# Optimization experiments

Measured on AMD Instinct MI355X. Metric: run time of the kernel, lower is better.

## Reference

```python
import jax, jax.numpy as jnp
import numpy as np

N = 20000      # nodes
E = 320000     # edges
F = 128        # feat_dim
N_RBF = 20
CUTOFF = 5.0


def setup_inputs() -> dict:
    key = jax.random.key(0)
    ks = jax.random.split(key, 12)
    h_i = jax.random.normal(ks[0], (N, F), dtype=jnp.float32)
    v_i = jax.random.normal(ks[1], (N, F, 3), dtype=jnp.float32)
    # distances in (0, cutoff); keep strictly > 0 to avoid div-by-zero in sinc basis
    d_ij = (jax.random.uniform(ks[2], (E,), dtype=jnp.float32) * 0.98 + 0.01) * CUTOFF
    r = jax.random.normal(ks[3], (E, 3), dtype=jnp.float32)
    unit_r_ij = r / jnp.linalg.norm(r, axis=-1, keepdims=True)
    nbrs = jax.random.randint(ks[4], (E, 2), 0, N, dtype=jnp.int64)
    # params: layers = Dense(F->F, swish) then Dense(F->3F); dist_embed dense: n_rbf -> 3F
    s1 = 1.0 / np.sqrt(F)
    W1 = jax.random.uniform(ks[5], (F, F), jnp.float32, -s1, s1)
    b1 = jax.random.uniform(ks[6], (F,), jnp.float32, -s1, s1)
    W2 = jax.random.uniform(ks[7], (F, 3 * F), jnp.float32, -s1, s1)
    b2 = jax.random.uniform(ks[8], (3 * F,), jnp.float32, -s1, s1)
    sr = 1.0 / np.sqrt(N_RBF)
    Wr = jax.random.uniform(ks[9], (N_RBF, 3 * F), jnp.float32, -sr, sr)
    br = jax.random.uniform(ks[10], (3 * F,), jnp.float32, -sr, sr)
    return {"h_i": h_i, "v_i": v_i, "d_ij": d_ij, "unit_r_ij": unit_r_ij,
            "nbrs": nbrs, "W1": W1, "b1": b1, "W2": W2, "b2": b2, "Wr": Wr, "br": br}


def _dist_embed(d, Wr, br):
    # PaiNN sinc-like radial basis: sin(n*pi*d/cutoff)/d, n=1..N_RBF
    n = jnp.arange(1, N_RBF + 1, dtype=d.dtype)
    rbf = jnp.sin(n[None, :] * jnp.pi * d[:, None] / CUTOFF) / d[:, None]  # [E, N_RBF]
    # cosine cutoff envelope
    fcut = 0.5 * (jnp.cos(jnp.pi * d / CUTOFF) + 1.0) * (d < CUTOFF)       # [E]
    return (rbf @ Wr + br) * fcut[:, None]                                  # [E, 3F]


def reference(h_i, v_i, d_ij, unit_r_ij, nbrs, W1, b1, W2, b2, Wr, br):
    # phi = Dense(swish) -> Dense : [N, 3F]
    phi = jax.nn.silu(h_i @ W1 + b1) @ W2 + b2
    src = nbrs[:, 1]
    dst = nbrs[:, 0]
    edge_inv = phi[src] * _dist_embed(d_ij, Wr, br)          # [E, 3F]
    edge_inv = edge_inv.reshape(edge_inv.shape[0], 3, F)     # [E, 3, F]
    f1, f2, f3 = edge_inv[:, 0], edge_inv[:, 1], edge_inv[:, 2]
    # dv: [E, F, 3]
    dv = f1[:, :, None] * unit_r_ij[:, None, :] + f2[:, :, None] * v_i[src]
    dh_i = jax.ops.segment_sum(f3, dst, num_segments=N)      # [N, F]
    dv_i = jax.ops.segment_sum(dv, dst, num_segments=N)      # [N, F, 3]
    return (dh_i, dv_i)
```

## Files before the change

kernel.cpp:

```cpp
#include <hip/hip_runtime.h>
#include <math.h>

#define F 128
#define THREEF 384
#define N_RBF 20
#define CUTOFF 5.0f
#define CAP 64
#define TLDS_STRIDE 136

typedef __bf16 bf16x8 __attribute__((ext_vector_type(8)));
typedef float  f32x4  __attribute__((ext_vector_type(4)));
typedef float  f32x2  __attribute__((ext_vector_type(2)));

__global__ __launch_bounds__(256) void init_kernel(
    const float* __restrict__ W1, const float* __restrict__ W2,
    const float* __restrict__ Wr,
    __bf16* __restrict__ W1T, __bf16* __restrict__ W2T,
    float* __restrict__ WrT, int* __restrict__ cnt, int N)
{
    const int tid = threadIdx.x;
    const int b   = blockIdx.x;

    if (b < 256) {
        const int idx = b * 256 + tid;
        if (idx < 128 * 128) {
            const int n = idx >> 7, k = idx & 127;
            W1T[idx] = (__bf16)W1[k * F + n];
        }
        if (idx < 384 * 128) {
            const int n = idx >> 7, k = idx & 127;
            W2T[idx] = (__bf16)W2[k * THREEF + n];
        }
    } else if (b < 264) {
        const int idx = (b - 256) * 256 + tid;
        if (idx >= 5 * 3 * 128) return;
        const int f  = idx & 127;
        const int c  = (idx >> 7) % 3;
        const int n4 = idx / (3 * 128);
        float4 v;
        v.x = Wr[(4 * n4 + 0) * THREEF + c * 128 + f];
        v.y = Wr[(4 * n4 + 1) * THREEF + c * 128 + f];
        v.z = Wr[(4 * n4 + 2) * THREEF + c * 128 + f];
        v.w = Wr[(4 * n4 + 3) * THREEF + c * 128 + f];
        ((float4*)WrT)[idx] = v;
    } else {
        const int i = (b - 264) * 256 + tid;
        if (i < (N + 3) / 4) {
            int4 z; z.x = 0; z.y = 0; z.z = 0; z.w = 0;
            ((int4*)cnt)[i] = z;
        }
    }
}

__global__ __launch_bounds__(256) void work_kernel(
    const float* __restrict__ d_ij, const float* __restrict__ unit_r,
    const int* __restrict__ nbrs,
    int* __restrict__ cnt, float* __restrict__ pack,
    const float* __restrict__ h,
    const __bf16* __restrict__ W1T, const float* __restrict__ b1,
    const __bf16* __restrict__ W2T, const float* __restrict__ b2,
    float* __restrict__ phi, int E, int EB, int N)
{
    __shared__ __bf16 t_lds[16 * TLDS_STRIDE];

    const int tid = threadIdx.x;
    const int b   = blockIdx.x;

    if (b < EB) {
        const int e = b * 256 + tid;
        if (e >= E) return;
        const int2 nb = ((const int2*)nbrs)[e];
        const int dst = nb.x;
        const int src = nb.y;
        const int slot = atomicAdd(&cnt[dst], 1);
        if (slot >= CAP) return;

        const float d = d_ij[e];
        const float x = (float)M_PI * d * (1.0f / CUTOFF);
        float sx, cx;
        __sincosf(x, &sx, &cx);
        const float fcut = (d < CUTOFF) ? 0.5f * (cx + 1.0f) : 0.0f;
        float4 q0, q1;
        q0.x = sx * fcut / d;
        q0.y = 2.0f * cx;
        q0.z = fcut;
        q0.w = unit_r[3 * e + 0];
        q1.x = unit_r[3 * e + 1];
        q1.y = unit_r[3 * e + 2];
        q1.z = __int_as_float(src);
        q1.w = 0.0f;
        float4* pk = (float4*)(pack + ((size_t)dst * CAP + slot) * 8);
        pk[0] = q0;
        pk[1] = q1;
        return;
    }

    const int wave = tid >> 6;
    const int lane = tid & 63;
    const int m    = lane & 15;
    const int quad = lane >> 4;
    const int node0 = (b - EB) * 16;
    if (node0 >= N) return;

    bf16x8 a1[4];
    #pragma unroll
    for (int kb = 0; kb < 4; ++kb) {
        const float* hp = h + (size_t)(node0 + m) * F + kb * 32 + quad * 8;
        const float4 x0 = *(const float4*)hp;
        const float4 x1 = *(const float4*)(hp + 4);
        bf16x8 a;
        a[0] = (__bf16)x0.x; a[1] = (__bf16)x0.y;
        a[2] = (__bf16)x0.z; a[3] = (__bf16)x0.w;
        a[4] = (__bf16)x1.x; a[5] = (__bf16)x1.y;
        a[6] = (__bf16)x1.z; a[7] = (__bf16)x1.w;
        a1[kb] = a;
    }

    #pragma unroll
    for (int c2 = 0; c2 < 2; ++c2) {
        const int ct = wave * 2 + c2;
        f32x4 acc = {0.0f, 0.0f, 0.0f, 0.0f};
        #pragma unroll
        for (int kb = 0; kb < 4; ++kb) {
            const bf16x8 bb =
                *(const bf16x8*)(W1T + (size_t)(ct * 16 + m) * F + kb * 32 + quad * 8);
            acc = __builtin_amdgcn_mfma_f32_16x16x32_bf16(a1[kb], bb, acc, 0, 0, 0);
        }
        const int col = ct * 16 + m;
        const float bb = b1[col];
        #pragma unroll
        for (int reg = 0; reg < 4; ++reg) {
            const float x = acc[reg] + bb;
            const float s = x / (1.0f + __expf(-x));
            t_lds[(quad * 4 + reg) * TLDS_STRIDE + col] = (__bf16)s;
        }
    }
    __syncthreads();

    bf16x8 a2[4];
    #pragma unroll
    for (int kb = 0; kb < 4; ++kb)
        a2[kb] = *(const bf16x8*)&t_lds[m * TLDS_STRIDE + kb * 32 + quad * 8];

    #pragma unroll
    for (int c6 = 0; c6 < 6; ++c6) {
        const int ct = c6 * 4 + wave;
        f32x4 acc = {0.0f, 0.0f, 0.0f, 0.0f};
        #pragma unroll
        for (int kb = 0; kb < 4; ++kb) {
            const bf16x8 bb =
                *(const bf16x8*)(W2T + (size_t)(ct * 16 + m) * F + kb * 32 + quad * 8);
            acc = __builtin_amdgcn_mfma_f32_16x16x32_bf16(a2[kb], bb, acc, 0, 0, 0);
        }
        const int col = ct * 16 + m;
        const float bb = b2[col];
        #pragma unroll
        for (int reg = 0; reg < 4; ++reg) {
            const int row = quad * 4 + reg;
            phi[(size_t)(node0 + row) * THREEF + col] = acc[reg] + bb;
        }
    }
}

__global__ __launch_bounds__(256)
__attribute__((amdgpu_waves_per_eu(2, 4)))
void gather_kernel(
    const float* __restrict__ phi,
    const float* __restrict__ v_i,
    const float* __restrict__ WrT,
    const float* __restrict__ br,
    const int*   __restrict__ cnt,
    const float* __restrict__ pack,
    float* __restrict__ dh,
    float* __restrict__ dv,
    int N)
{
    __shared__ float4 s_pack[2][CAP * 2];

    const int tid  = threadIdx.x;
    const int half = tid >> 7;
    const int f    = tid & 127;
    const int node = blockIdx.x * 2 + half;

    const int deg0 = cnt[node];
    const int deg  = deg0 < CAP ? deg0 : CAP;
    const int degR = (deg + 3) & ~3;

    {
        const float4* srcp = (const float4*)(pack + (size_t)node * CAP * 8);
        if (f < 2 * degR) {
            float4 v = make_float4(0.0f, 0.0f, 0.0f, 0.0f);
            if (f < 2 * deg) v = srcp[f];
            s_pack[half][f] = v;
        }
    }
    __syncthreads();

    const float br0 = br[f], br1 = br[f + 128], br2 = br[f + 256];
    const f32x4* wT = (const f32x4*)WrT;

    float dh_acc = 0.0f, dvx = 0.0f, dvy = 0.0f, dvz = 0.0f;

    for (int i0 = 0; i0 < degR; i0 += 4) {
        float s1[4], twoc[4], fcut[4], ux[4], uy[4], uz[4];
        float ph0[4], ph1[4], ph2[4], vx[4], vy[4], vz[4];
        #pragma unroll
        for (int j = 0; j < 4; ++j) {
            const float4 q0 = s_pack[half][2 * (i0 + j)];
            const float4 q1 = s_pack[half][2 * (i0 + j) + 1];
            s1[j] = q0.x; twoc[j] = q0.y; fcut[j] = q0.z;
            ux[j] = q0.w; uy[j] = q1.x;   uz[j] = q1.y;
            const int src = __builtin_amdgcn_readfirstlane(__float_as_int(q1.z));
            const float* pp = phi + (size_t)src * THREEF + f;
            ph0[j] = pp[0];  ph1[j] = pp[128]; ph2[j] = pp[256];
            const float* vs = v_i + (size_t)src * THREEF + 3 * f;
            vx[j] = vs[0];   vy[j] = vs[1];    vz[j] = vs[2];
        }

        f32x2 t2[4], rc[4], rp[4], A0[4], A1[4], A2[4];
        #pragma unroll
        for (int j = 0; j < 4; ++j) {
            const float t2s = fmaf(twoc[j], twoc[j], -2.0f);
            t2[j][0] = t2s;      t2[j][1] = t2s;
            rc[j][0] = s1[j];    rc[j][1] = twoc[j] * s1[j];
            rp[j][0] = -s1[j];   rp[j][1] = 0.0f;
            A0[j] = (f32x2){0.0f, 0.0f};
            A1[j] = (f32x2){0.0f, 0.0f};
            A2[j] = (f32x2){0.0f, 0.0f};
        }

        #pragma unroll
        for (int n4 = 0; n4 < 5; ++n4) {
            const f32x4 w0 = wT[(n4 * 3 + 0) * 128 + f];
            const f32x4 w1 = wT[(n4 * 3 + 1) * 128 + f];
            const f32x4 w2 = wT[(n4 * 3 + 2) * 128 + f];
            const f32x2 w0lo = __builtin_shufflevector(w0, w0, 0, 1);
            const f32x2 w1lo = __builtin_shufflevector(w1, w1, 0, 1);
            const f32x2 w2lo = __builtin_shufflevector(w2, w2, 0, 1);
            const f32x2 w0hi = __builtin_shufflevector(w0, w0, 2, 3);
            const f32x2 w1hi = __builtin_shufflevector(w1, w1, 2, 3);
            const f32x2 w2hi = __builtin_shufflevector(w2, w2, 2, 3);
            #pragma unroll
            for (int j = 0; j < 4; ++j) {
                A0[j] = __builtin_elementwise_fma(rc[j], w0lo, A0[j]);
                A1[j] = __builtin_elementwise_fma(rc[j], w1lo, A1[j]);
                A2[j] = __builtin_elementwise_fma(rc[j], w2lo, A2[j]);
                f32x2 rn = __builtin_elementwise_fma(t2[j], rc[j], -rp[j]);
                rp[j] = rc[j]; rc[j] = rn;
                A0[j] = __builtin_elementwise_fma(rc[j], w0hi, A0[j]);
                A1[j] = __builtin_elementwise_fma(rc[j], w1hi, A1[j]);
                A2[j] = __builtin_elementwise_fma(rc[j], w2hi, A2[j]);
                rn = __builtin_elementwise_fma(t2[j], rc[j], -rp[j]);
                rp[j] = rc[j]; rc[j] = rn;
            }
        }

        #pragma unroll
        for (int j = 0; j < 4; ++j) {
            const float a0 = fmaf(br0, fcut[j], A0[j][0] + A0[j][1]);
            const float a1 = fmaf(br1, fcut[j], A1[j][0] + A1[j][1]);
            const float a2 = fmaf(br2, fcut[j], A2[j][0] + A2[j][1]);
            const float f1 = ph0[j] * a0;
            const float f2 = ph1[j] * a1;
            const float f3 = ph2[j] * a2;
            dh_acc += f3;
            dvx = fmaf(f1, ux[j], fmaf(f2, vx[j], dvx));
            dvy = fmaf(f1, uy[j], fmaf(f2, vy[j], dvy));
            dvz = fmaf(f1, uz[j], fmaf(f2, vz[j], dvz));
        }
    }

    dh[(size_t)node * F + f] = dh_acc;
    float* dvp = dv + (size_t)node * THREEF + 3 * f;
    dvp[0] = dvx;
    dvp[1] = dvy;
    dvp[2] = dvz;
}

extern "C" void kernel_launch(void* const* d_in, const int* in_sizes, int n_in,
                              void* d_out, int out_size, void* d_ws, size_t ws_size,
                              hipStream_t stream) {
    const float* h_i    = (const float*)d_in[0];
    const float* v_i    = (const float*)d_in[1];
    const float* d_ij   = (const float*)d_in[2];
    const float* unit_r = (const float*)d_in[3];
    const int*   nbrs   = (const int*)  d_in[4];
    const float* W1     = (const float*)d_in[5];
    const float* b1     = (const float*)d_in[6];
    const float* W2     = (const float*)d_in[7];
    const float* b2     = (const float*)d_in[8];
    const float* Wr     = (const float*)d_in[9];
    const float* br     = (const float*)d_in[10];

    const int N = in_sizes[0] / F;
    const int E = in_sizes[2];

    float* dh = (float*)d_out;
    float* dv = dh + (size_t)N * F;

    float*  phi  = (float*)d_ws;
    float*  pack = phi + (size_t)3 * N * F;
    float*  WrT  = pack + (size_t)N * CAP * 8;
    int*    cnt  = (int*)(WrT + 5 * 3 * 128 * 4);
    __bf16* W1T  = (__bf16*)(cnt + N);
    __bf16* W2T  = W1T + 128 * 128;

    const int EB = (E + 255) / 256;
    const int MB = (N + 15) / 16;
    const int ZB = ((N + 3) / 4 + 255) / 256;

    init_kernel<<<256 + 8 + ZB, 256, 0, stream>>>(W1, W2, Wr, W1T, W2T, WrT,
                                                  cnt, N);
    work_kernel<<<EB + MB, 256, 0, stream>>>(d_ij, unit_r, nbrs, cnt, pack,
                                             h_i, W1T, b1, W2T, b2, phi,
                                             E, EB, N);
    gather_kernel<<<N / 2, 256, 0, stream>>>(phi, v_i, WrT, br, cnt, pack,
                                             dh, dv, N);
}
```

Before: 281.0 us.

## Pack phi and v_i into interleaved fp16 per-node gather buffer

The MLP output phi and the node vectors v_i are now stored together as fp16 in a single per-node buffer, with the six values for each feature interleaved. The gather kernel reads three 32-bit words per source and feature instead of six scattered fp32 loads. A new block range in work_kernel converts v_i into this buffer. The aim is to halve the bytes gathered per edge and keep the gathered values contiguous, at the cost of fp16 rounding of phi and v_i and an extra conversion pass over v_i.

```diff
diff --git a/kernel.cpp b/kernel.cpp
--- a/kernel.cpp
+++ b/kernel.cpp
@@ -11,6 +11,16 @@
 typedef __bf16 bf16x8 __attribute__((ext_vector_type(8)));
 typedef float  f32x4  __attribute__((ext_vector_type(4)));
 typedef float  f32x2  __attribute__((ext_vector_type(2)));
+typedef _Float16 f16x2 __attribute__((ext_vector_type(2)));
+
+static __device__ __forceinline__ float loh(unsigned int u) {
+    const f16x2 h = __builtin_bit_cast(f16x2, u);
+    return (float)h[0];
+}
+static __device__ __forceinline__ float hih(unsigned int u) {
+    const f16x2 h = __builtin_bit_cast(f16x2, u);
+    return (float)h[1];
+}
 
 __global__ __launch_bounds__(256) void init_kernel(
     const float* __restrict__ W1, const float* __restrict__ W2,
@@ -54,12 +64,12 @@
 
 __global__ __launch_bounds__(256) void work_kernel(
     const float* __restrict__ d_ij, const float* __restrict__ unit_r,
-    const int* __restrict__ nbrs,
+    const int* __restrict__ nbrs, const float* __restrict__ v_i,
     int* __restrict__ cnt, float* __restrict__ pack,
     const float* __restrict__ h,
     const __bf16* __restrict__ W1T, const float* __restrict__ b1,
     const __bf16* __restrict__ W2T, const float* __restrict__ b2,
-    float* __restrict__ phi, int E, int EB, int N)
+    _Float16* __restrict__ gh, int E, int EB, int MB, int N)
 {
     __shared__ __bf16 t_lds[16 * TLDS_STRIDE];
 
@@ -95,6 +105,18 @@
         return;
     }
 
+    if (b >= EB + MB) {
+        const int idx = (b - EB - MB) * 256 + tid;
+        if (idx >= N * F) return;
+        const int node = idx >> 7, f = idx & 127;
+        const float* vs = v_i + (size_t)node * THREEF + 3 * f;
+        _Float16* gp = gh + (size_t)node * 768 + 6 * f + 3;
+        gp[0] = (_Float16)vs[0];
+        gp[1] = (_Float16)vs[1];
+        gp[2] = (_Float16)vs[2];
+        return;
+    }
+
     const int wave = tid >> 6;
     const int lane = tid & 63;
     const int m    = lane & 15;
@@ -152,12 +174,15 @@
                 *(const bf16x8*)(W2T + (size_t)(ct * 16 + m) * F + kb * 32 + quad * 8);
             acc = __builtin_amdgcn_mfma_f32_16x16x32_bf16(a2[kb], bb, acc, 0, 0, 0);
         }
-        const int col = ct * 16 + m;
-        const float bb = b2[col];
+        const int col   = ct * 16 + m;
+        const int plane = col >> 7;
+        const int fc    = col & 127;
+        const float bb  = b2[col];
         #pragma unroll
         for (int reg = 0; reg < 4; ++reg) {
             const int row = quad * 4 + reg;
-            phi[(size_t)(node0 + row) * THREEF + col] = acc[reg] + bb;
+            gh[(size_t)(node0 + row) * 768 + 6 * fc + plane] =
+                (_Float16)(acc[reg] + bb);
         }
     }
 }
@@ -165,8 +190,7 @@
 __global__ __launch_bounds__(256)
 __attribute__((amdgpu_waves_per_eu(2, 4)))
 void gather_kernel(
-    const float* __restrict__ phi,
-    const float* __restrict__ v_i,
+    const _Float16* __restrict__ gh,
     const float* __restrict__ WrT,
     const float* __restrict__ br,
     const int*   __restrict__ cnt,
@@ -211,10 +235,12 @@
             s1[j] = q0.x; twoc[j] = q0.y; fcut[j] = q0.z;
             ux[j] = q0.w; uy[j] = q1.x;   uz[j] = q1.y;
             const int src = __builtin_amdgcn_readfirstlane(__float_as_int(q1.z));
-            const float* pp = phi + (size_t)src * THREEF + f;
-            ph0[j] = pp[0];  ph1[j] = pp[128]; ph2[j] = pp[256];
-            const float* vs = v_i + (size_t)src * THREEF + 3 * f;
-            vx[j] = vs[0];   vy[j] = vs[1];    vz[j] = vs[2];
+            const unsigned int* gb =
+                (const unsigned int*)(gh + (size_t)src * 768) + 3 * f;
+            const unsigned int d0 = gb[0], d1 = gb[1], d2 = gb[2];
+            ph0[j] = loh(d0); ph1[j] = hih(d0);
+            ph2[j] = loh(d1); vx[j]  = hih(d1);
+            vy[j]  = loh(d2); vz[j]  = hih(d2);
         }
 
         f32x2 t2[4], rc[4], rp[4], A0[4], A1[4], A2[4];
@@ -298,8 +324,9 @@
     float* dh = (float*)d_out;
     float* dv = dh + (size_t)N * F;
 
-    float*  phi  = (float*)d_ws;
-    float*  pack = phi + (size_t)3 * N * F;
+    _Float16* gh  = (_Float16*)d_ws;
+    float*  pack = (float*)d_ws + (size_t)3 * N * F / 2 + N * F / 2;
+    pack = (float*)((char*)d_ws + (size_t)N * 768 * sizeof(_Float16));
     float*  WrT  = pack + (size_t)N * CAP * 8;
     int*    cnt  = (int*)(WrT + 5 * 3 * 128 * 4);
     __bf16* W1T  = (__bf16*)(cnt + N);
@@ -307,13 +334,14 @@
 
     const int EB = (E + 255) / 256;
     const int MB = (N + 15) / 16;
+    const int VB = (N * F + 255) / 256;
     const int ZB = ((N + 3) / 4 + 255) / 256;
 
     init_kernel<<<256 + 8 + ZB, 256, 0, stream>>>(W1, W2, Wr, W1T, W2T, WrT,
                                                   cnt, N);
-    work_kernel<<<EB + MB, 256, 0, stream>>>(d_ij, unit_r, nbrs, cnt, pack,
-                                             h_i, W1T, b1, W2T, b2, phi,
-                                             E, EB, N);
-    gather_kernel<<<N / 2, 256, 0, stream>>>(phi, v_i, WrT, br, cnt, pack,
+    work_kernel<<<EB + MB + VB, 256, 0, stream>>>(d_ij, unit_r, nbrs, v_i,
+                                                  cnt, pack, h_i, W1T, b1,
+                                                  W2T, b2, gh, E, EB, MB, N);
+    gather_kernel<<<N / 2, 256, 0, stream>>>(gh, WrT, br, cnt, pack,
                                              dh, dv, N);
 }
```

New measurement: 269.5 us. 4.1% less time.
